# Optimization experiments

Measured on AMD Instinct MI355X. Metric: run time of the kernel, lower is better.

Reference implementation:

```python
import jax, jax.numpy as jnp
import numpy as np

NUM_HEADS = 16
INPUT_SIZE = 1024
KEY_SIZE = 64
VALUE_SIZE = 64
LN_EPS = 1e-5


def setup_inputs() -> dict:
    key = jax.random.key(0)
    ks = jax.random.split(key, 11)
    B, S, D = 2, 2048, INPUT_SIZE
    Hk = NUM_HEADS * KEY_SIZE
    Hv = NUM_HEADS * VALUE_SIZE
    s = 0.02
    return {
        "queries": jax.random.normal(ks[0], (B, S, D), dtype=jnp.float32),
        "Wq": jax.random.normal(ks[1], (D, Hk), dtype=jnp.float32) * s,
        "bq": jnp.zeros((Hk,), dtype=jnp.float32),
        "Wk": jax.random.normal(ks[2], (D, Hk), dtype=jnp.float32) * s,
        "bk": jnp.zeros((Hk,), dtype=jnp.float32),
        "Wv": jax.random.normal(ks[3], (D, Hv), dtype=jnp.float32) * s,
        "bv": jnp.zeros((Hv,), dtype=jnp.float32),
        "Wo": jax.random.normal(ks[4], (Hv, D), dtype=jnp.float32) * s,
        "bo": jnp.zeros((D,), dtype=jnp.float32),
        "ln_gamma": jnp.ones((D,), dtype=jnp.float32),
        "ln_beta": jnp.zeros((D,), dtype=jnp.float32),
    }


def reference(queries, Wq, bq, Wk, bk, Wv, bv, Wo, bo, ln_gamma, ln_beta):
    B, S, D = queries.shape
    H, dk, dv = NUM_HEADS, KEY_SIZE, VALUE_SIZE
    residual = queries
    # projections -> [B, S, H, d]
    q = (queries @ Wq + bq).reshape(B, S, H, dk)
    k = (queries @ Wk + bk).reshape(B, S, H, dk)
    v = (queries @ Wv + bv).reshape(B, S, H, dv)
    # scaled dot-product attention per head
    scores = jnp.einsum("bqhd,bkhd->bhqk", q, k) / jnp.sqrt(jnp.float32(dk))
    attn = jax.nn.softmax(scores, axis=-1)
    out = jnp.einsum("bhqk,bkhd->bqhd", attn, v).reshape(B, S, H * dv)
    # out projection + residual + layernorm (dropout=0 / eval)
    res = out @ Wo + bo + residual
    mu = jnp.mean(res, axis=-1, keepdims=True)
    var = jnp.var(res, axis=-1, keepdims=True)
    return (res - mu) / jnp.sqrt(var + LN_EPS) * ln_gamma + ln_beta
```

## Files before the change

kernel.cpp:

```cpp
#include <hip/hip_runtime.h>
#include <hip/hip_bf16.h>
#include <math.h>

#define D 1024
#define NH 16
#define DK 64
#define LN_EPS 1e-5f
typedef __hip_bfloat16 bf16;
typedef __attribute__((ext_vector_type(8))) short bf16x8;
typedef __attribute__((ext_vector_type(4))) short short4v;
typedef __attribute__((ext_vector_type(4))) float f32x4;
typedef __attribute__((ext_vector_type(2))) unsigned int uint2v;

__device__ inline float tofloat(bf16 x) { return __bfloat162float(x); }
__device__ inline float tofs(short s) {
    bf16 b; __builtin_memcpy(&b, &s, 2);
    return __bfloat162float(b);
}
__device__ inline unsigned int pk2(float a, float b) {
    float2 f2; f2.x = a; f2.y = b;
    __hip_bfloat162 h = __float22bfloat162_rn(f2);
    unsigned int u; __builtin_memcpy(&u, &h, 4);
    return u;
}
__device__ inline short4v pk4(float a, float b, float c, float d) {
    uint2v u; u[0] = pk2(a, b); u[1] = pk2(c, d);
    short4v s; __builtin_memcpy(&s, &u, 8);
    return s;
}
__device__ inline bf16x8 pk8(const float* f) {
    uint2v a, b;
    a[0] = pk2(f[0], f[1]); a[1] = pk2(f[2], f[3]);
    b[0] = pk2(f[4], f[5]); b[1] = pk2(f[6], f[7]);
    bf16x8 o;
    short4v s0, s1;
    __builtin_memcpy(&s0, &a, 8); __builtin_memcpy(&s1, &b, 8);
#pragma unroll
    for (int i = 0; i < 4; ++i) { o[i] = s0[i]; o[4 + i] = s1[i]; }
    return o;
}

__device__ inline int wave_isf32(const unsigned short* __restrict__ Xu) {
    unsigned short u = Xu[threadIdx.x & 63];
    unsigned long long m = __ballot(((u >> 7) & 0xFF) >= 0x90);
    return __popcll(m) > 2;
}

__global__ void prep_kernel(const void* X, const void* Wq, const void* Wk, const void* Wv,
                            const void* Wo, const void* bq, const void* bk, const void* bv,
                            const void* bo, const void* g, const void* be,
                            bf16* __restrict__ Xb, bf16* __restrict__ Wqkvt, bf16* __restrict__ Wot,
                            bf16* __restrict__ bqkv, bf16* __restrict__ bob,
                            bf16* __restrict__ gb, bf16* __restrict__ beb) {
    __shared__ float tile[64][65];
    const int isf32 = wave_isf32((const unsigned short*)X);
    const int bid = blockIdx.x;
    const int tid = threadIdx.x;
    if (bid < 2048) {
        int e0 = bid * 2048 + tid * 8;
        bf16x8 outv;
        if (isf32) {
            float4 v0 = ((const float4*)X)[e0 / 4];
            float4 v1 = ((const float4*)X)[e0 / 4 + 1];
            float f[8] = {v0.x, v0.y, v0.z, v0.w, v1.x, v1.y, v1.z, v1.w};
            outv = pk8(f);
        } else {
            outv = ((const bf16x8*)X)[e0 / 8];
        }
        *(bf16x8*)(Xb + e0) = outv;
    } else if (bid < 3072) {
        int t = bid - 2048;
        int z = t >> 8, rem = t & 255;
        const void* srcs[4] = {Wq, Wk, Wv, Wo};
        const void* src = srcs[z];
        bf16* dst = (z < 3) ? (Wqkvt + (size_t)z * 1024 * 1024) : Wot;
        const int i0 = (rem >> 4) * 64, j0 = (rem & 15) * 64;
        const int tr = tid >> 4, tc4 = (tid & 15) * 4;
#pragma unroll
        for (int p = 0; p < 4; ++p) {
            int r = p * 16 + tr;
            if (isf32) {
                float4 v = *(const float4*)((const float*)src + (size_t)(i0 + r) * 1024 + j0 + tc4);
                tile[r][tc4] = v.x; tile[r][tc4 + 1] = v.y;
                tile[r][tc4 + 2] = v.z; tile[r][tc4 + 3] = v.w;
            } else {
                short4v v = *(const short4v*)((const bf16*)src + (size_t)(i0 + r) * 1024 + j0 + tc4);
#pragma unroll
                for (int q = 0; q < 4; ++q) tile[r][tc4 + q] = tofs(v[q]);
            }
        }
        __syncthreads();
        const int wj = tid >> 3, wi = (tid & 7) * 8;
#pragma unroll
        for (int p = 0; p < 2; ++p) {
            int j = p * 32 + wj;
            float f[8];
#pragma unroll
            for (int q = 0; q < 8; ++q) f[q] = tile[wi + q][j];
            *(bf16x8*)(dst + (size_t)(j0 + j) * 1024 + i0 + wi) = pk8(f);
        }
    } else {
        int idx = (bid - 3072) * 256 + tid;
        int seg = idx >> 10, off = idx & 1023;
        const void* srcs[6] = {bq, bk, bv, bo, g, be};
        const void* src = srcs[seg];
        float v = isf32 ? ((const float*)src)[off] : tofloat(((const bf16*)src)[off]);
        bf16 bv16 = __float2bfloat16(v);
        if (seg < 3)       bqkv[seg * 1024 + off] = bv16;
        else if (seg == 3) bob[off] = bv16;
        else if (seg == 4) gb[off] = bv16;
        else               beb[off] = bv16;
    }
}

__global__ __launch_bounds__(256) void gemm_qkv(const bf16* __restrict__ A, const bf16* __restrict__ Bt,
                                                const bf16* __restrict__ bias,
                                                bf16* __restrict__ C, bf16* __restrict__ VtG,
                                                int M, int N, int K, int S) {
    __shared__ short As[128][72];
    __shared__ short Bs[128][72];
    const int tid = threadIdx.x;
    const int lane = tid & 63, wave = tid >> 6;
    const int wy = wave >> 1, wx = wave & 1;
    const int mrow = lane & 15, quad = lane >> 4;
    const int lb = blockIdx.y * gridDim.x + blockIdx.x;
    const int xcd = lb & 7, j = lb >> 3;
    const int bm = (xcd * 4 + (j & 3)) * 128;
    const int bn = (j >> 2) * 128;

    f32x4 acc[4][4];
#pragma unroll
    for (int mi = 0; mi < 4; ++mi)
#pragma unroll
        for (int nt = 0; nt < 4; ++nt) acc[mi][nt] = (f32x4){0.f, 0.f, 0.f, 0.f};

    const int ra = tid >> 1, ca = (tid & 1) * 32;
    const bf16* aptr = A + (size_t)(bm + ra) * K + ca;
    const bf16* bptr = Bt + (size_t)(bn + ra) * K + ca;
    bf16x8 ar0, ar1, ar2, ar3, br0, br1, br2, br3;
    ar0 = *(const bf16x8*)(aptr);      ar1 = *(const bf16x8*)(aptr + 8);
    ar2 = *(const bf16x8*)(aptr + 16); ar3 = *(const bf16x8*)(aptr + 24);
    br0 = *(const bf16x8*)(bptr);      br1 = *(const bf16x8*)(bptr + 8);
    br2 = *(const bf16x8*)(bptr + 16); br3 = *(const bf16x8*)(bptr + 24);

    for (int k0 = 0; k0 < K; k0 += 64) {
        __syncthreads();
        *(bf16x8*)&As[ra][ca] = ar0;      *(bf16x8*)&As[ra][ca + 8] = ar1;
        *(bf16x8*)&As[ra][ca + 16] = ar2; *(bf16x8*)&As[ra][ca + 24] = ar3;
        *(bf16x8*)&Bs[ra][ca] = br0;      *(bf16x8*)&Bs[ra][ca + 8] = br1;
        *(bf16x8*)&Bs[ra][ca + 16] = br2; *(bf16x8*)&Bs[ra][ca + 24] = br3;
        __syncthreads();
        if (k0 + 64 < K) {
            ar0 = *(const bf16x8*)(aptr + k0 + 64);      ar1 = *(const bf16x8*)(aptr + k0 + 72);
            ar2 = *(const bf16x8*)(aptr + k0 + 80);      ar3 = *(const bf16x8*)(aptr + k0 + 88);
            br0 = *(const bf16x8*)(bptr + k0 + 64);      br1 = *(const bf16x8*)(bptr + k0 + 72);
            br2 = *(const bf16x8*)(bptr + k0 + 80);      br3 = *(const bf16x8*)(bptr + k0 + 88);
        }
#pragma unroll
        for (int ks = 0; ks < 2; ++ks) {
            bf16x8 a[4], b[4];
#pragma unroll
            for (int mi = 0; mi < 4; ++mi)
                a[mi] = *(const bf16x8*)&As[wy * 64 + mi * 16 + mrow][ks * 32 + quad * 8];
#pragma unroll
            for (int nt = 0; nt < 4; ++nt)
                b[nt] = *(const bf16x8*)&Bs[wx * 64 + nt * 16 + mrow][ks * 32 + quad * 8];
#pragma unroll
            for (int mi = 0; mi < 4; ++mi)
#pragma unroll
                for (int nt = 0; nt < 4; ++nt)
                    acc[mi][nt] = __builtin_amdgcn_mfma_f32_16x16x32_bf16(a[mi], b[nt], acc[mi][nt], 0, 0, 0);
        }
    }
#pragma unroll
    for (int mi = 0; mi < 4; ++mi) {
#pragma unroll
        for (int nt = 0; nt < 4; ++nt) {
            int col = bn + wx * 64 + nt * 16 + mrow;
            float bc = tofloat(bias[col]);
            if (col >= 2048) {
                int dvf = col - 2048, hh = dvf >> 6, dv = dvf & 63;
                int row0 = bm + wy * 64 + mi * 16 + quad * 4;
                int bb = row0 / S, key0 = row0 % S;
                short4v pk = pk4(acc[mi][nt][0] + bc, acc[mi][nt][1] + bc,
                                 acc[mi][nt][2] + bc, acc[mi][nt][3] + bc);
                *(short4v*)(VtG + (size_t)(bb * NH + hh) * S * 64 + (key0 >> 2) * 256 + dv * 4) = pk;
            } else {
                float sc = (col < 1024) ? 0.18033688f : 1.0f;
#pragma unroll
                for (int reg = 0; reg < 4; ++reg) {
                    int row = bm + wy * 64 + mi * 16 + quad * 4 + reg;
                    C[(size_t)row * N + col] = __float2bfloat16((acc[mi][nt][reg] + bc) * sc);
                }
            }
        }
    }
}

__global__ __launch_bounds__(256) void gemm_out(const bf16* __restrict__ A, const bf16* __restrict__ Bt,
                                                const bf16* __restrict__ bias,
                                                const bf16* __restrict__ residual,
                                                float* __restrict__ C, int M, int N, int K) {
    __shared__ short As[128][72];
    __shared__ short Bs[64][72];
    const int tid = threadIdx.x;
    const int lane = tid & 63, wave = tid >> 6;
    const int wy = wave >> 1, wx = wave & 1;
    const int mrow = lane & 15, quad = lane >> 4;
    const int lb = blockIdx.y * gridDim.x + blockIdx.x;
    const int xcd = lb & 7, j = lb >> 3;
    const int bm = (xcd * 4 + (j & 3)) * 128;
    const int bn = (j >> 2) * 64;

    f32x4 acc[4][2];
#pragma unroll
    for (int mi = 0; mi < 4; ++mi)
#pragma unroll
        for (int nt = 0; nt < 2; ++nt) acc[mi][nt] = (f32x4){0.f, 0.f, 0.f, 0.f};

    const int ra = tid >> 1, ca = (tid & 1) * 32;
    const int rb = tid >> 2, cb = (tid & 3) * 16;
    const bf16* aptr = A + (size_t)(bm + ra) * K + ca;
    const bf16* bptr = Bt + (size_t)(bn + rb) * K + cb;
    bf16x8 ar0, ar1, ar2, ar3, br0, br1;
    ar0 = *(const bf16x8*)(aptr);      ar1 = *(const bf16x8*)(aptr + 8);
    ar2 = *(const bf16x8*)(aptr + 16); ar3 = *(const bf16x8*)(aptr + 24);
    br0 = *(const bf16x8*)(bptr);      br1 = *(const bf16x8*)(bptr + 8);

    for (int k0 = 0; k0 < K; k0 += 64) {
        __syncthreads();
        *(bf16x8*)&As[ra][ca] = ar0;      *(bf16x8*)&As[ra][ca + 8] = ar1;
        *(bf16x8*)&As[ra][ca + 16] = ar2; *(bf16x8*)&As[ra][ca + 24] = ar3;
        *(bf16x8*)&Bs[rb][cb] = br0;      *(bf16x8*)&Bs[rb][cb + 8] = br1;
        __syncthreads();
        if (k0 + 64 < K) {
            ar0 = *(const bf16x8*)(aptr + k0 + 64); ar1 = *(const bf16x8*)(aptr + k0 + 72);
            ar2 = *(const bf16x8*)(aptr + k0 + 80); ar3 = *(const bf16x8*)(aptr + k0 + 88);
            br0 = *(const bf16x8*)(bptr + k0 + 64); br1 = *(const bf16x8*)(bptr + k0 + 72);
        }
#pragma unroll
        for (int ks = 0; ks < 2; ++ks) {
            bf16x8 a[4], b[2];
#pragma unroll
            for (int mi = 0; mi < 4; ++mi)
                a[mi] = *(const bf16x8*)&As[wy * 64 + mi * 16 + mrow][ks * 32 + quad * 8];
#pragma unroll
            for (int nt = 0; nt < 2; ++nt)
                b[nt] = *(const bf16x8*)&Bs[wx * 32 + nt * 16 + mrow][ks * 32 + quad * 8];
#pragma unroll
            for (int mi = 0; mi < 4; ++mi)
#pragma unroll
                for (int nt = 0; nt < 2; ++nt)
                    acc[mi][nt] = __builtin_amdgcn_mfma_f32_16x16x32_bf16(a[mi], b[nt], acc[mi][nt], 0, 0, 0);
        }
    }
#pragma unroll
    for (int mi = 0; mi < 4; ++mi) {
#pragma unroll
        for (int nt = 0; nt < 2; ++nt) {
            int col = bn + wx * 32 + nt * 16 + mrow;
            float bc = tofloat(bias[col]);
#pragma unroll
            for (int reg = 0; reg < 4; ++reg) {
                int row = bm + wy * 64 + mi * 16 + quad * 4 + reg;
                C[(size_t)row * N + col] = acc[mi][nt][reg] + bc + tofloat(residual[(size_t)row * N + col]);
            }
        }
    }
}

__global__ __launch_bounds__(256, 3) void attn_mfma(const bf16* __restrict__ QKV,
                                                    const bf16* __restrict__ VtG,
                                                    bf16* __restrict__ Ob, int S, int M) {
    __shared__ short Ks[2][64][72];
    __shared__ short Vs2[2][16 * 256];
    const int tid = threadIdx.x;
    const int lane = tid & 63, wave = tid >> 6;
    const int mrow = lane & 15, quad = lane >> 4;
    const int ldq = 3 * D;
    const int lb = blockIdx.y * gridDim.x + blockIdx.x;
    const int xcd = lb & 7, idx = lb >> 3;
    const int bh = xcd * 4 + (idx >> 4);
    const int qc = idx & 15;
    const int b = bh / NH, h = bh % NH;
    const int q0 = qc * 128 + wave * 32;

    bf16x8 qf[2][2];
#pragma unroll
    for (int qt = 0; qt < 2; ++qt) {
        const bf16* qbase = QKV + ((size_t)(b * S + q0 + qt * 16 + mrow)) * ldq + h * DK;
        qf[qt][0] = *(const bf16x8*)(qbase + quad * 8);
        qf[qt][1] = *(const bf16x8*)(qbase + 32 + quad * 8);
    }

    f32x4 o[2][4];
#pragma unroll
    for (int qt = 0; qt < 2; ++qt)
#pragma unroll
        for (int t = 0; t < 4; ++t) o[qt][t] = (f32x4){0.f, 0.f, 0.f, 0.f};
    float lsum[2] = {0.f, 0.f};

    const int rs_ = tid >> 2, cs_ = (tid & 3) * 16;
    const bf16* kb0 = QKV + ((size_t)(b * S + rs_)) * ldq + D + h * DK + cs_;
    const bf16* vb0 = VtG + (size_t)(b * NH + h) * S * 64 + tid * 16;
    const int kg_l = tid >> 4, dv0 = (tid & 15) * 4;
    const int voff = kg_l * 256 + (((dv0 + kg_l * 8) & 63) * 4);

    {
        bf16x8 k0v = *(const bf16x8*)kb0, k1v = *(const bf16x8*)(kb0 + 8);
        bf16x8 v0v = *(const bf16x8*)vb0, v1v = *(const bf16x8*)(vb0 + 8);
        *(bf16x8*)&Ks[0][rs_][cs_] = k0v;
        *(bf16x8*)&Ks[0][rs_][cs_ + 8] = k1v;
        *(bf16x8*)&Vs2[0][voff] = v0v;
        *(bf16x8*)&Vs2[0][voff + 8] = v1v;
    }

    for (int kc = 0; kc < S; kc += 64) {
        const int cur = (kc >> 6) & 1;
        __syncthreads();
        bf16x8 kr0, kr1, vr0, vr1;
        const int more = (kc + 64 < S);
        if (more) {
            const bf16* kn = kb0 + (size_t)(kc + 64) * ldq;
            kr0 = *(const bf16x8*)kn; kr1 = *(const bf16x8*)(kn + 8);
            const bf16* vn = vb0 + (size_t)(kc + 64) * 64;
            vr0 = *(const bf16x8*)vn; vr1 = *(const bf16x8*)(vn + 8);
        }

        f32x4 s[2][4];
#pragma unroll
        for (int qt = 0; qt < 2; ++qt)
#pragma unroll
            for (int t = 0; t < 4; ++t) s[qt][t] = (f32x4){0.f, 0.f, 0.f, 0.f};
        __builtin_amdgcn_s_setprio(1);
#pragma unroll
        for (int ks = 0; ks < 2; ++ks) {
#pragma unroll
            for (int t = 0; t < 4; ++t) {
                bf16x8 kf = *(const bf16x8*)&Ks[cur][t * 16 + mrow][ks * 32 + quad * 8];
                s[0][t] = __builtin_amdgcn_mfma_f32_16x16x32_bf16(kf, qf[0][ks], s[0][t], 0, 0, 0);
                s[1][t] = __builtin_amdgcn_mfma_f32_16x16x32_bf16(kf, qf[1][ks], s[1][t], 0, 0, 0);
            }
        }
        __builtin_amdgcn_s_setprio(0);
        short4v pf[2][4];
#pragma unroll
        for (int qt = 0; qt < 2; ++qt)
#pragma unroll
            for (int t = 0; t < 4; ++t) {
                float p0 = __builtin_amdgcn_exp2f(s[qt][t][0]);
                float p1 = __builtin_amdgcn_exp2f(s[qt][t][1]);
                float p2 = __builtin_amdgcn_exp2f(s[qt][t][2]);
                float p3 = __builtin_amdgcn_exp2f(s[qt][t][3]);
                lsum[qt] += (p0 + p1) + (p2 + p3);
                pf[qt][t] = pk4(p0, p1, p2, p3);
            }
        __builtin_amdgcn_s_setprio(1);
#pragma unroll
        for (int kt = 0; kt < 4; ++kt) {
            const int kg = kt * 4 + quad;
#pragma unroll
            for (int dvt = 0; dvt < 4; ++dvt) {
                int dvs = ((dvt * 16 + mrow) + kg * 8) & 63;
                short4v vf = *(const short4v*)&Vs2[cur][kg * 256 + dvs * 4];
                o[0][dvt] = __builtin_amdgcn_mfma_f32_16x16x16bf16_1k(pf[0][kt], vf, o[0][dvt], 0, 0, 0);
                o[1][dvt] = __builtin_amdgcn_mfma_f32_16x16x16bf16_1k(pf[1][kt], vf, o[1][dvt], 0, 0, 0);
            }
        }
        __builtin_amdgcn_s_setprio(0);
        if (more) {
            *(bf16x8*)&Ks[cur ^ 1][rs_][cs_] = kr0;
            *(bf16x8*)&Ks[cur ^ 1][rs_][cs_ + 8] = kr1;
            *(bf16x8*)&Vs2[cur ^ 1][voff] = vr0;
            *(bf16x8*)&Vs2[cur ^ 1][voff + 8] = vr1;
        }
    }
#pragma unroll
    for (int qt = 0; qt < 2; ++qt) {
        float v = lsum[qt];
        v += __shfl_xor(v, 16, 64);
        v += __shfl_xor(v, 32, 64);
        lsum[qt] = v;
    }
#pragma unroll
    for (int qt = 0; qt < 2; ++qt)
#pragma unroll
        for (int r = 0; r < 4; ++r) {
            float inv = 1.0f / __shfl(lsum[qt], quad * 4 + r, 64);
            bf16* orow = Ob + ((size_t)(b * S + q0 + qt * 16 + quad * 4 + r)) * D + h * DK;
#pragma unroll
            for (int dvt = 0; dvt < 4; ++dvt)
                orow[dvt * 16 + mrow] = __float2bfloat16(o[qt][dvt][r] * inv);
        }
}

__global__ void ln_kernel(const float* __restrict__ R, const bf16* __restrict__ gamma,
                          const bf16* __restrict__ beta, void* __restrict__ out,
                          const void* __restrict__ X) {
    __shared__ float red[8];
    const int isf32 = wave_isf32((const unsigned short*)X);
    const int row = blockIdx.x;
    const float4 xv = *(const float4*)(R + (size_t)row * D + threadIdx.x * 4);
    float sum = xv.x + xv.y + xv.z + xv.w;
    float sq = xv.x * xv.x + xv.y * xv.y + xv.z * xv.z + xv.w * xv.w;
    for (int off = 32; off; off >>= 1) {
        sum += __shfl_xor(sum, off, 64);
        sq += __shfl_xor(sq, off, 64);
    }
    const int wave = threadIdx.x / 64, lane = threadIdx.x % 64;
    if (lane == 0) { red[wave] = sum; red[wave + 4] = sq; }
    __syncthreads();
    sum = red[0] + red[1] + red[2] + red[3];
    sq = red[4] + red[5] + red[6] + red[7];
    const float mu = sum / (float)D;
    const float var = sq / (float)D - mu * mu;
    const float inv = rsqrtf(var + LN_EPS);
    const float x4[4] = {xv.x, xv.y, xv.z, xv.w};
#pragma unroll
    for (int i = 0; i < 4; ++i) {
        int cidx = threadIdx.x * 4 + i;
        float y = (x4[i] - mu) * inv * tofloat(gamma[cidx]) + tofloat(beta[cidx]);
        size_t oidx = (size_t)row * D + cidx;
        if (isf32) ((float*)out)[oidx] = y;
        else       ((bf16*)out)[oidx] = __float2bfloat16(y);
    }
}

extern "C" void kernel_launch(void* const* d_in, const int* in_sizes, int n_in,
                              void* d_out, int out_size, void* d_ws, size_t ws_size,
                              hipStream_t stream) {
    const int M = in_sizes[0] / D;
    const int B = 2;
    const int S = M / B;

    char* p = (char*)d_ws;
    auto alloc = [&](size_t bytes) { char* r = p; p += (bytes + 255) & ~(size_t)255; return r; };
    bf16* Xb    = (bf16*)alloc((size_t)M * D * 2);
    bf16* Wqkvt = (bf16*)alloc((size_t)3 * D * D * 2);
    bf16* Wot   = (bf16*)alloc((size_t)D * D * 2);
    bf16* bqkv  = (bf16*)alloc(3 * D * 2);
    bf16* bob   = (bf16*)alloc(D * 2);
    bf16* gb    = (bf16*)alloc(D * 2);
    bf16* beb   = (bf16*)alloc(D * 2);
    bf16* QKV   = (bf16*)alloc((size_t)M * 3 * D * 2);
    bf16* VtG   = (bf16*)alloc((size_t)M * D * 2);
    bf16* Ob    = (bf16*)alloc((size_t)M * D * 2);
    float* Rf   = (float*)alloc((size_t)M * D * 4);

    prep_kernel<<<3096, 256, 0, stream>>>(d_in[0], d_in[1], d_in[3], d_in[5], d_in[7],
                                          d_in[2], d_in[4], d_in[6], d_in[8], d_in[9], d_in[10],
                                          Xb, Wqkvt, Wot, bqkv, bob, gb, beb);

    gemm_qkv<<<dim3(3 * D / 128, M / 128), 256, 0, stream>>>(
        Xb, Wqkvt, bqkv, QKV, VtG, M, 3 * D, D, S);

    attn_mfma<<<dim3(B * NH * (S / 128)), 256, 0, stream>>>(QKV, VtG, Ob, S, M);

    gemm_out<<<dim3(D / 64, M / 128), 256, 0, stream>>>(Ob, Wot, bob, Xb, Rf, M, D, D);

    ln_kernel<<<M, 256, 0, stream>>>(Rf, gb, beb, d_out, d_in[0]);
}
```

Before: 211.0 us.

## Load GEMM tiles directly into LDS with XOR-swizzled layout

```diff
diff --git a/kernel.cpp b/kernel.cpp
--- a/kernel.cpp
+++ b/kernel.cpp
@@ -38,6 +38,11 @@
 #pragma unroll
     for (int i = 0; i < 4; ++i) { o[i] = s0[i]; o[4 + i] = s1[i]; }
     return o;
+}
+
+__device__ inline void gload16(const bf16* g, void* l) {
+    __builtin_amdgcn_global_load_lds((const __attribute__((address_space(1))) void*)g,
+                                     (__attribute__((address_space(3))) void*)l, 16, 0, 0);
 }
 
 __device__ inline int wave_isf32(const unsigned short* __restrict__ Xu) {
@@ -117,8 +122,8 @@
                                                 const bf16* __restrict__ bias,
                                                 bf16* __restrict__ C, bf16* __restrict__ VtG,
                                                 int M, int N, int K, int S) {
-    __shared__ short As[128][72];
-    __shared__ short Bs[128][72];
+    __shared__ short As[128 * 64];
+    __shared__ short Bs[128 * 64];
     const int tid = threadIdx.x;
     const int lane = tid & 63, wave = tid >> 6;
     const int wy = wave >> 1, wx = wave & 1;
@@ -134,37 +139,33 @@
 #pragma unroll
         for (int nt = 0; nt < 4; ++nt) acc[mi][nt] = (f32x4){0.f, 0.f, 0.f, 0.f};
 
-    const int ra = tid >> 1, ca = (tid & 1) * 32;
-    const bf16* aptr = A + (size_t)(bm + ra) * K + ca;
-    const bf16* bptr = Bt + (size_t)(bn + ra) * K + ca;
-    bf16x8 ar0, ar1, ar2, ar3, br0, br1, br2, br3;
-    ar0 = *(const bf16x8*)(aptr);      ar1 = *(const bf16x8*)(aptr + 8);
-    ar2 = *(const bf16x8*)(aptr + 16); ar3 = *(const bf16x8*)(aptr + 24);
-    br0 = *(const bf16x8*)(bptr);      br1 = *(const bf16x8*)(bptr + 8);
-    br2 = *(const bf16x8*)(bptr + 16); br3 = *(const bf16x8*)(bptr + 24);
+    const int l8 = lane >> 3;
+    const int sx = (lane & 7) ^ l8;
+    const bf16* ag = A + (size_t)(bm + wave * 32 + l8) * K + sx * 8;
+    const bf16* bg = Bt + (size_t)(bn + wave * 32 + l8) * K + sx * 8;
+    char* asl = (char*)As + wave * 4096;
+    char* bsl = (char*)Bs + wave * 4096;
+    const int rxor = (mrow & 7) << 4;
 
     for (int k0 = 0; k0 < K; k0 += 64) {
         __syncthreads();
-        *(bf16x8*)&As[ra][ca] = ar0;      *(bf16x8*)&As[ra][ca + 8] = ar1;
-        *(bf16x8*)&As[ra][ca + 16] = ar2; *(bf16x8*)&As[ra][ca + 24] = ar3;
-        *(bf16x8*)&Bs[ra][ca] = br0;      *(bf16x8*)&Bs[ra][ca + 8] = br1;
-        *(bf16x8*)&Bs[ra][ca + 16] = br2; *(bf16x8*)&Bs[ra][ca + 24] = br3;
-        __syncthreads();
-        if (k0 + 64 < K) {
-            ar0 = *(const bf16x8*)(aptr + k0 + 64);      ar1 = *(const bf16x8*)(aptr + k0 + 72);
-            ar2 = *(const bf16x8*)(aptr + k0 + 80);      ar3 = *(const bf16x8*)(aptr + k0 + 88);
-            br0 = *(const bf16x8*)(bptr + k0 + 64);      br1 = *(const bf16x8*)(bptr + k0 + 72);
-            br2 = *(const bf16x8*)(bptr + k0 + 80);      br3 = *(const bf16x8*)(bptr + k0 + 88);
-        }
+#pragma unroll
+        for (int i = 0; i < 4; ++i) {
+            gload16(ag + (size_t)i * 8 * K + k0, asl + i * 1024);
+            gload16(bg + (size_t)i * 8 * K + k0, bsl + i * 1024);
+        }
+        __syncthreads();
 #pragma unroll
         for (int ks = 0; ks < 2; ++ks) {
             bf16x8 a[4], b[4];
 #pragma unroll
             for (int mi = 0; mi < 4; ++mi)
-                a[mi] = *(const bf16x8*)&As[wy * 64 + mi * 16 + mrow][ks * 32 + quad * 8];
+                a[mi] = *(const bf16x8*)((const char*)As +
+                         (wy * 64 + mi * 16 + mrow) * 128 + ((ks * 64 + quad * 16) ^ rxor));
 #pragma unroll
             for (int nt = 0; nt < 4; ++nt)
-                b[nt] = *(const bf16x8*)&Bs[wx * 64 + nt * 16 + mrow][ks * 32 + quad * 8];
+                b[nt] = *(const bf16x8*)((const char*)Bs +
+                         (wx * 64 + nt * 16 + mrow) * 128 + ((ks * 64 + quad * 16) ^ rxor));
 #pragma unroll
             for (int mi = 0; mi < 4; ++mi)
 #pragma unroll
@@ -201,8 +202,8 @@
                                                 const bf16* __restrict__ bias,
                                                 const bf16* __restrict__ residual,
                                                 float* __restrict__ C, int M, int N, int K) {
-    __shared__ short As[128][72];
-    __shared__ short Bs[64][72];
+    __shared__ short As[128 * 64];
+    __shared__ short Bs[64 * 64];
     const int tid = threadIdx.x;
     const int lane = tid & 63, wave = tid >> 6;
     const int wy = wave >> 1, wx = wave & 1;
@@ -218,35 +219,34 @@
 #pragma unroll
         for (int nt = 0; nt < 2; ++nt) acc[mi][nt] = (f32x4){0.f, 0.f, 0.f, 0.f};
 
-    const int ra = tid >> 1, ca = (tid & 1) * 32;
-    const int rb = tid >> 2, cb = (tid & 3) * 16;
-    const bf16* aptr = A + (size_t)(bm + ra) * K + ca;
-    const bf16* bptr = Bt + (size_t)(bn + rb) * K + cb;
-    bf16x8 ar0, ar1, ar2, ar3, br0, br1;
-    ar0 = *(const bf16x8*)(aptr);      ar1 = *(const bf16x8*)(aptr + 8);
-    ar2 = *(const bf16x8*)(aptr + 16); ar3 = *(const bf16x8*)(aptr + 24);
-    br0 = *(const bf16x8*)(bptr);      br1 = *(const bf16x8*)(bptr + 8);
+    const int l8 = lane >> 3;
+    const int sx = (lane & 7) ^ l8;
+    const bf16* ag = A + (size_t)(bm + wave * 32 + l8) * K + sx * 8;
+    const bf16* bg = Bt + (size_t)(bn + wave * 16 + l8) * K + sx * 8;
+    char* asl = (char*)As + wave * 4096;
+    char* bsl = (char*)Bs + wave * 2048;
+    const int rxor = (mrow & 7) << 4;
 
     for (int k0 = 0; k0 < K; k0 += 64) {
         __syncthreads();
-        *(bf16x8*)&As[ra][ca] = ar0;      *(bf16x8*)&As[ra][ca + 8] = ar1;
-        *(bf16x8*)&As[ra][ca + 16] = ar2; *(bf16x8*)&As[ra][ca + 24] = ar3;
-        *(bf16x8*)&Bs[rb][cb] = br0;      *(bf16x8*)&Bs[rb][cb + 8] = br1;
-        __syncthreads();
-        if (k0 + 64 < K) {
-            ar0 = *(const bf16x8*)(aptr + k0 + 64); ar1 = *(const bf16x8*)(aptr + k0 + 72);
-            ar2 = *(const bf16x8*)(aptr + k0 + 80); ar3 = *(const bf16x8*)(aptr + k0 + 88);
-            br0 = *(const bf16x8*)(bptr + k0 + 64); br1 = *(const bf16x8*)(bptr + k0 + 72);
-        }
+#pragma unroll
+        for (int i = 0; i < 4; ++i)
+            gload16(ag + (size_t)i * 8 * K + k0, asl + i * 1024);
+#pragma unroll
+        for (int i = 0; i < 2; ++i)
+            gload16(bg + (size_t)i * 8 * K + k0, bsl + i * 1024);
+        __syncthreads();
 #pragma unroll
         for (int ks = 0; ks < 2; ++ks) {
             bf16x8 a[4], b[2];
 #pragma unroll
             for (int mi = 0; mi < 4; ++mi)
-                a[mi] = *(const bf16x8*)&As[wy * 64 + mi * 16 + mrow][ks * 32 + quad * 8];
+                a[mi] = *(const bf16x8*)((const char*)As +
+                         (wy * 64 + mi * 16 + mrow) * 128 + ((ks * 64 + quad * 16) ^ rxor));
 #pragma unroll
             for (int nt = 0; nt < 2; ++nt)
-                b[nt] = *(const bf16x8*)&Bs[wx * 32 + nt * 16 + mrow][ks * 32 + quad * 8];
+                b[nt] = *(const bf16x8*)((const char*)Bs +
+                         (wx * 32 + nt * 16 + mrow) * 128 + ((ks * 64 + quad * 16) ^ rxor));
 #pragma unroll
             for (int mi = 0; mi < 4; ++mi)
 #pragma unroll
@@ -278,7 +278,7 @@
     const int lane = tid & 63, wave = tid >> 6;
     const int mrow = lane & 15, quad = lane >> 4;
     const int ldq = 3 * D;
-    const int lb = blockIdx.y * gridDim.x + blockIdx.x;
+    const int lb = blockIdx.x;
     const int xcd = lb & 7, idx = lb >> 3;
     const int bh = xcd * 4 + (idx >> 4);
     const int qc = idx & 15;
```

Result: no change. 213.3 us (+1.1%).
